# Kernel tuning notes

Hardware: AMD Instinct MI355X
Metric: run time of the kernel (lower is better)

Reference implementation:

```python
import jax, jax.numpy as jnp
import numpy as np

B, N, C, K = 8, 4096, 64, 30
EPS_BN = 1e-5
TINY = 1e-20  # guards sqrt/atan2 at the exact self-neighbor (rel == 0)


def _knn(p, k):
    xx = jnp.sum(p * p, axis=1)  # [B, N]
    pd = 2.0 * jnp.einsum('bdn,bdm->bnm', p, p) - xx[:, :, None] - xx[:, None, :]
    return jax.lax.top_k(pd, k)[1]  # [B, N, k]


def _bn(h, g, b):
    # BatchNorm1d in training mode: biased batch stats over all dims but channel (last)
    mu = jnp.mean(h, axis=(0, 1, 2), keepdims=True)
    var = jnp.var(h, axis=(0, 1, 2), keepdims=True)
    return (h - mu) * jax.lax.rsqrt(var + EPS_BN) * g + b


def _forward(x_loc, x, W1, g1, b1, W2, g2, b2, W3, g3, b3, k):
    Bsz = x.shape[0]
    idx = _knn(x_loc, k)                       # [B, N, k]
    bidx = jnp.arange(Bsz)[:, None, None]
    pts = x_loc.transpose(0, 2, 1)             # [B, N, 3]
    rel = pts[bidx, idx] - pts[:, :, None, :]  # [B, N, k, 3] neighbor - center
    xr, yr, zr = rel[..., 0], rel[..., 1], rel[..., 2]
    sxy2 = xr * xr + yr * yr
    r2 = sxy2 + zr * zr
    rho = jnp.sqrt(jnp.maximum(r2, TINY))
    sxy = jnp.sqrt(jnp.maximum(sxy2, TINY))
    deg_r = r2 < TINY
    deg_p = sxy2 < TINY
    theta = jnp.arctan2(jnp.where(deg_r, 0.0, zr), jnp.where(deg_r, 1.0, sxy))
    phi = jnp.arctan2(jnp.where(deg_p, 0.0, yr), jnp.where(deg_p, 1.0, xr))
    sph = jnp.stack([rho, theta, phi], axis=-1)            # [B, N, k, 3]
    # torch car2sph averages across the 3 spherical channels (dim=-1)
    feat = jnp.concatenate([sph, sph - jnp.mean(sph, axis=-1, keepdims=True)], axis=-1)  # [B,N,k,6]
    lrelu = lambda h: jax.nn.leaky_relu(h, 0.2)
    h = lrelu(_bn(feat @ W1.T, g1, b1))        # [B, N, k, 6]
    h = lrelu(_bn(h @ W2.T, g2, b2))           # [B, N, k, 3]
    h = lrelu(_bn(h @ W3.T, g3, b3))           # [B, N, k, 1]
    att = jax.nn.softmax(h[..., 0], axis=-1)   # [B, N, k]
    xk = x.transpose(0, 2, 1)[bidx, idx]       # [B, N, k, C]
    agg = jnp.einsum('bnkc,bnk->bnc', xk, att)
    return x + agg.transpose(0, 2, 1)          # [B, C, N]


def setup_inputs() -> dict:
    key = jax.random.key(0)
    ks = jax.random.split(key, 12)
    return {
        'x_loc': jax.random.normal(ks[0], (B, 3, N), jnp.float32),
        'x': jax.random.normal(ks[1], (B, C, N), jnp.float32),
        'W1': jax.random.normal(ks[2], (6, 6), jnp.float32) * 0.4,
        'g1': 1.0 + 0.1 * jax.random.normal(ks[3], (6,), jnp.float32),
        'b1': 0.1 * jax.random.normal(ks[4], (6,), jnp.float32),
        'W2': jax.random.normal(ks[5], (3, 6), jnp.float32) * 0.4,
        'g2': 1.0 + 0.1 * jax.random.normal(ks[6], (3,), jnp.float32),
        'b2': 0.1 * jax.random.normal(ks[7], (3,), jnp.float32),
        'W3': jax.random.normal(ks[8], (1, 3), jnp.float32) * 0.4,
        'g3': 1.0 + 0.1 * jax.random.normal(ks[9], (1,), jnp.float32),
        'b3': 0.1 * jax.random.normal(ks[10], (1,), jnp.float32),
        'k': K,
    }


def reference(x_loc, x, W1, g1, b1, W2, g2, b2, W3, g3, b3, k):
    return _forward(x_loc, x, W1, g1, b1, W2, g2, b2, W3, g3, b3, k)
```

## Files before the change

kernel.cpp:

```cpp
#include <hip/hip_runtime.h>
#include <math.h>

#define NPTS 4096
#define NB   8
#define NC   64
#define KSEL 30
#define NROWS (NB * NPTS * KSEL)
#define CNT_F 983040.0f
#define SURVZ 3840
#define P23_BLOCKS 960
#define P23_STRIDE (P23_BLOCKS * 256)

static __device__ __forceinline__ unsigned long long shfl_xor_u64(unsigned long long v, int lx) {
    int lo = __shfl_xor((int)(unsigned)(v & 0xFFFFFFFFULL), lx, 64);
    int hi = __shfl_xor((int)(unsigned)(v >> 32), lx, 64);
    return ((unsigned long long)(unsigned)hi << 32) | (unsigned)lo;
}

template <int NM>
static __device__ __forceinline__ void slot_reduce(const float* __restrict__ acc,
                                                   float* __restrict__ sSum, int tid) {
    if (tid < 64) {
        float pm[NM];
#pragma unroll
        for (int m = 0; m < NM; ++m) pm[m] = acc[m * 64 + tid];
#pragma unroll
        for (int o = 32; o > 0; o >>= 1) {
#pragma unroll
            for (int m = 0; m < NM; ++m) pm[m] += __shfl_xor(pm[m], o, 64);
        }
        if (tid == 0) {
#pragma unroll
            for (int m = 0; m < NM; ++m) sSum[m] = pm[m];
        }
    }
}

static __device__ __forceinline__ void bn1_params(const float* __restrict__ sSum,
                                                  const float* __restrict__ W1,
                                                  const float* __restrict__ g1,
                                                  const float* __restrict__ b1,
                                                  float* __restrict__ sPar, int tid) {
    if (tid < 6) {
        const float invN = 1.0f / CNT_F;
        const float m0 = sSum[0] * invN, m1 = sSum[1] * invN, m2 = sSum[2] * invN;
        const float E00 = sSum[3] * invN, E01 = sSum[4] * invN, E02 = sSum[5] * invN;
        const float E11 = sSum[6] * invN, E12 = sSum[7] * invN, E22 = sSum[8] * invN;
        const float* w = W1 + tid * 6;
        const float third = (w[3] + w[4] + w[5]) * (1.0f / 3.0f);
        const float a0 = w[0] + w[3] - third;
        const float a1 = w[1] + w[4] - third;
        const float a2 = w[2] + w[5] - third;
        const float mu = a0 * m0 + a1 * m1 + a2 * m2;
        const float E2 = a0 * a0 * E00 + a1 * a1 * E11 + a2 * a2 * E22 +
                         2.0f * (a0 * a1 * E01 + a0 * a2 * E02 + a1 * a2 * E12);
        const float var = E2 - mu * mu;
        const float sc = g1[tid] / sqrtf(var + 1e-5f);
        sPar[tid] = sc;
        sPar[6 + tid] = b1[tid] - mu * sc;
    }
}

static __device__ __forceinline__ void bn2_params(const float* __restrict__ sSum,
                                                  const float* __restrict__ W2,
                                                  const float* __restrict__ g2,
                                                  const float* __restrict__ b2,
                                                  float* __restrict__ sPar, int tid) {
    if (tid < 3) {
        const float invN = 1.0f / CNT_F;
        float Eh[6];
#pragma unroll
        for (int d = 0; d < 6; ++d) Eh[d] = sSum[d] * invN;
        float M[6][6];
        int q = 6;
#pragma unroll
        for (int a2 = 0; a2 < 6; ++a2)
#pragma unroll
            for (int b2_ = a2; b2_ < 6; ++b2_) {
                const float v = sSum[q++] * invN;
                M[a2][b2_] = v; M[b2_][a2] = v;
            }
        const float* w = W2 + tid * 6;
        float mu = 0.0f;
#pragma unroll
        for (int d = 0; d < 6; ++d) mu += w[d] * Eh[d];
        float E2 = 0.0f;
#pragma unroll
        for (int a2 = 0; a2 < 6; ++a2)
#pragma unroll
            for (int b2_ = 0; b2_ < 6; ++b2_) E2 += w[a2] * w[b2_] * M[a2][b2_];
        const float var = E2 - mu * mu;
        const float sc = g2[tid] / sqrtf(var + 1e-5f);
        sPar[12 + tid] = sc;
        sPar[15 + tid] = b2[tid] - mu * sc;
    }
}

static __device__ __forceinline__ void bn3_params(const float* __restrict__ sSum,
                                                  const float* __restrict__ W3,
                                                  const float* __restrict__ g3,
                                                  const float* __restrict__ b3,
                                                  float* __restrict__ sPar, int tid) {
    if (tid == 0) {
        const float invN = 1.0f / CNT_F;
        const float Eh0 = sSum[0] * invN, Eh1 = sSum[1] * invN, Eh2 = sSum[2] * invN;
        const float M00 = sSum[3] * invN, M01 = sSum[4] * invN, M02 = sSum[5] * invN;
        const float M11 = sSum[6] * invN, M12 = sSum[7] * invN, M22 = sSum[8] * invN;
        const float w0 = W3[0], w1 = W3[1], w2 = W3[2];
        const float mu = w0 * Eh0 + w1 * Eh1 + w2 * Eh2;
        const float E2 = w0 * w0 * M00 + w1 * w1 * M11 + w2 * w2 * M22 +
                         2.0f * (w0 * w1 * M01 + w0 * w2 * M02 + w1 * w2 * M12);
        const float var = E2 - mu * mu;
        const float sc = g3[0] / sqrtf(var + 1e-5f);
        sPar[0] = sc;
        sPar[1] = b3[0] - mu * sc;
    }
}

static __device__ __forceinline__ void mlp_h1(float s0, float s1, float s2,
                                              const float* __restrict__ W1,
                                              const float* __restrict__ sPar,
                                              float* __restrict__ h1) {
    const float mean = (s0 + s1 + s2) * (1.0f / 3.0f);
    const float f[6] = {s0, s1, s2, s0 - mean, s1 - mean, s2 - mean};
#pragma unroll
    for (int c = 0; c < 6; ++c) {
        float a = 0.0f;
#pragma unroll
        for (int d = 0; d < 6; ++d) a = fmaf(W1[c * 6 + d], f[d], a);
        const float z = fmaf(a, sPar[c], sPar[6 + c]);
        h1[c] = z >= 0.0f ? z : 0.2f * z;
    }
}

static __device__ __forceinline__ void mlp_h2(const float* __restrict__ h1,
                                              const float* __restrict__ W2,
                                              const float* __restrict__ sPar,
                                              float* __restrict__ h2) {
#pragma unroll
    for (int c = 0; c < 3; ++c) {
        float a = 0.0f;
#pragma unroll
        for (int d = 0; d < 6; ++d) a = fmaf(W2[c * 6 + d], h1[d], a);
        const float z = fmaf(a, sPar[12 + c], sPar[15 + c]);
        h2[c] = z >= 0.0f ? z : 0.2f * z;
    }
}

__global__ __launch_bounds__(512, 4) void knn_k(const float* __restrict__ xloc,
                                                int* __restrict__ idx_out,
                                                float* __restrict__ sph,
                                                float* __restrict__ accM) {
    __shared__ float4 pts[NPTS];
    __shared__ float msc[72];

    const int tid  = threadIdx.x;
    const int lane = tid & 63;
    const int wv   = tid >> 6;
    const int b    = blockIdx.y;
    const int n    = (blockIdx.x << 3) + wv;

    const float* xb = xloc + (size_t)b * (3 * NPTS);
    for (int i = tid; i < NPTS; i += 512) {
        const float x = xb[i], y = xb[NPTS + i], z = xb[2 * NPTS + i];
        const float xx = __fadd_rn(__fadd_rn(__fmul_rn(x, x), __fmul_rn(y, y)), __fmul_rn(z, z));
        pts[i] = make_float4(x, y, z, xx);
    }
    __syncthreads();

    const float4 q = pts[n];

    unsigned K[64];
    unsigned lm = 0;
#pragma unroll
    for (int t = 0; t < 64; ++t) {
        const float4 c = pts[lane + (t << 6)];
        const float dt = __fadd_rn(__fadd_rn(__fmul_rn(q.x, c.x), __fmul_rn(q.y, c.y)), __fmul_rn(q.z, c.z));
        const float pd = __fsub_rn(__fsub_rn(__fmul_rn(2.0f, dt), q.w), c.w);
        const unsigned u = __float_as_uint(pd);
        const unsigned key = u ^ ((unsigned)((int)u >> 31) | 0x80000000u);
        K[t] = key;
        lm = key > lm ? key : lm;
    }

    unsigned v = lm;
#pragma unroll
    for (int k = 2; k <= 64; k <<= 1) {
#pragma unroll
        for (int j2 = k >> 1; j2 > 0; j2 >>= 1) {
            const unsigned o = (unsigned)__shfl_xor((int)v, j2, 64);
            const bool keepmax = ((lane & j2) == 0) == ((lane & k) == 0);
            const unsigned mx = v > o ? v : o;
            const unsigned mn = v > o ? o : v;
            v = keepmax ? mx : mn;
        }
    }
    const unsigned tau = (unsigned)__shfl((int)v, 30, 64);

    __syncthreads();

    unsigned long long* surv = ((unsigned long long*)(pts + SURVZ)) + (wv << 6);
    surv[lane] = 0ULL;

    unsigned total = 0;
#pragma unroll
    for (int t = 0; t < 64; ++t) {
        const bool p = (K[t] >= tau);
        const unsigned long long m = __ballot(p);
        if (p) {
            const unsigned pos = total + (unsigned)__popcll(m & ((1ULL << lane) - 1ULL));
            if (pos < 64u) {
                const unsigned j = (unsigned)(lane + (t << 6));
                surv[pos] = ((unsigned long long)K[t] << 32) | (unsigned)(~j);
            }
        }
        total += (unsigned)__popcll(m);
    }
    __threadfence_block();

    const int bn = (b << 12) + n;
    const size_t obase = (size_t)bn * KSEL;
    int jn = 0;

    if (total <= 64u) {
        unsigned long long s = surv[lane];
#pragma unroll
        for (int k = 2; k <= 64; k <<= 1) {
#pragma unroll
            for (int j2 = k >> 1; j2 > 0; j2 >>= 1) {
                const unsigned long long o = shfl_xor_u64(s, j2);
                const bool keepmax = ((lane & j2) == 0) == ((lane & k) == 0);
                const unsigned long long mx = s > o ? s : o;
                const unsigned long long mn = s > o ? o : s;
                s = keepmax ? mx : mn;
            }
        }
        jn = (int)(~(unsigned)s) & (NPTS - 1);
        if (lane >= KSEL) jn = 0;
    } else {
        unsigned P = 0;
        for (int bit = 31; bit >= 0; --bit) {
            const unsigned cand = P | (1u << bit);
            int c = 0;
#pragma unroll
            for (int t = 0; t < 64; ++t) c += (K[t] >= cand) ? 1 : 0;
#pragma unroll
            for (int o = 32; o > 0; o >>= 1) c += __shfl_xor(c, o, 64);
            if (c >= KSEL) P = cand;
        }
        int* sj = (int*)surv;
        int emitted = 0;
#pragma unroll
        for (int t = 0; t < 64; ++t) {
            const bool g = (K[t] > P);
            const unsigned long long m = __ballot(g);
            if (g) {
                const int pos = emitted + (int)__popcll(m & ((1ULL << lane) - 1ULL));
                if (pos < KSEL) sj[pos] = lane + (t << 6);
            }
            emitted += (int)__popcll(m);
        }
#pragma unroll
        for (int t = 0; t < 64; ++t) {
            const bool e_ = (K[t] == P);
            const unsigned long long m = __ballot(e_);
            const int before = (int)__popcll(m & ((1ULL << lane) - 1ULL));
            if (e_ && (emitted + before) < KSEL) sj[emitted + before] = lane + (t << 6);
            emitted += (int)__popcll(m);
        }
        __threadfence_block();
        if (lane < KSEL) jn = sj[lane];
    }

    float s0 = 0.0f, s1 = 0.0f, s2 = 0.0f;
    if (lane < KSEL) {
        idx_out[obase + lane] = jn;
        float cx, cy, cz;
        if (jn >= SURVZ) {
            cx = xb[jn]; cy = xb[NPTS + jn]; cz = xb[2 * NPTS + jn];
        } else {
            const float4 c = pts[jn];
            cx = c.x; cy = c.y; cz = c.z;
        }
        const float xr = cx - q.x, yr = cy - q.y, zr = cz - q.z;
        const float sxy2 = xr * xr + yr * yr;
        const float r2   = sxy2 + zr * zr;
        const float rho  = sqrtf(fmaxf(r2, 1e-20f));
        const float sxy  = sqrtf(fmaxf(sxy2, 1e-20f));
        const bool dr = r2 < 1e-20f;
        const bool dp = sxy2 < 1e-20f;
        const float theta = atan2f(dr ? 0.0f : zr, dr ? 1.0f : sxy);
        const float phi   = atan2f(dp ? 0.0f : yr, dp ? 1.0f : xr);
        sph[obase + lane]             = rho;
        sph[NROWS + obase + lane]     = theta;
        sph[2 * NROWS + obase + lane] = phi;
        s0 = rho; s1 = theta; s2 = phi;
    }

    float mom[9] = {s0, s1, s2, s0 * s0, s0 * s1, s0 * s2, s1 * s1, s1 * s2, s2 * s2};
#pragma unroll
    for (int o = 32; o > 0; o >>= 1) {
#pragma unroll
        for (int m = 0; m < 9; ++m) mom[m] += __shfl_xor(mom[m], o, 64);
    }
    if (lane == 0) {
#pragma unroll
        for (int m = 0; m < 9; ++m) msc[wv * 9 + m] = mom[m];
    }
    __syncthreads();
    if (tid < 9) {
        float t_ = 0.0f;
#pragma unroll
        for (int w = 0; w < 8; ++w) t_ += msc[w * 9 + tid];
        atomicAdd(&accM[tid * 64 + ((blockIdx.y * 512 + blockIdx.x) & 63)], t_);
    }
}

__global__ __launch_bounds__(256) void p2_k(const float* __restrict__ sph,
                                            const float* __restrict__ x,
                                            float* __restrict__ xT,
                                            const float* __restrict__ W1,
                                            const float* __restrict__ g1,
                                            const float* __restrict__ b1,
                                            const float* __restrict__ accM,
                                            float* __restrict__ acc2) {
    __shared__ float sSum[9];
    __shared__ float sPar[12];
    __shared__ float red[4][27];
    __shared__ float tile[64][65];
    const int tid = threadIdx.x;
    slot_reduce<9>(accM, sSum, tid);
    __syncthreads();
    bn1_params(sSum, W1, g1, b1, sPar, tid);
    __syncthreads();

    float m27[27];
#pragma unroll
    for (int m = 0; m < 27; ++m) m27[m] = 0.0f;
#pragma unroll
    for (int s = 0; s < 4; ++s) {
        const size_t r = (size_t)blockIdx.x * 256 + tid + (size_t)s * P23_STRIDE;
        const float s0 = sph[r], s1 = sph[NROWS + r], s2 = sph[2 * NROWS + r];
        float h1[6];
        mlp_h1(s0, s1, s2, W1, sPar, h1);
        int qq = 6;
#pragma unroll
        for (int a2 = 0; a2 < 6; ++a2) {
            m27[a2] += h1[a2];
#pragma unroll
            for (int b2_ = a2; b2_ < 6; ++b2_) m27[qq++] += h1[a2] * h1[b2_];
        }
    }
#pragma unroll
    for (int o = 32; o > 0; o >>= 1) {
#pragma unroll
        for (int m = 0; m < 27; ++m) m27[m] += __shfl_xor(m27[m], o, 64);
    }
    const int lane = tid & 63, wv = tid >> 6;
    if (lane == 0) {
#pragma unroll
        for (int m = 0; m < 27; ++m) red[wv][m] = m27[m];
    }
    __syncthreads();
    if (tid < 27) {
        const float v = red[0][tid] + red[1][tid] + red[2][tid] + red[3][tid];
        atomicAdd(&acc2[tid * 64 + (blockIdx.x & 63)], v);
    }

    if (blockIdx.x < 512) {
        const int b  = blockIdx.x >> 6;
        const int n0 = (blockIdx.x & 63) << 6;
        const int tx = tid & 63;
        const int ty = tid >> 6;
        const float* xb = x + ((size_t)b << 18);
#pragma unroll
        for (int i = 0; i < 16; ++i) {
            const int c = (i << 2) + ty;
            tile[c][tx] = xb[((size_t)c << 12) + n0 + tx];
        }
        __syncthreads();
        float* ob = xT + ((size_t)b << 18);
#pragma unroll
        for (int i = 0; i < 16; ++i) {
            const int nl = (i << 2) + ty;
            ob[((size_t)(n0 + nl) << 6) + tx] = tile[tx][nl];
        }
    }
}

__global__ __launch_bounds__(256) void p3_k(const float* __restrict__ sph,
                                            const float* __restrict__ W1,
                                            const float* __restrict__ g1,
                                            const float* __restrict__ b1,
                                            const float* __restrict__ W2,
                                            const float* __restrict__ g2,
                                            const float* __restrict__ b2,
                                            const float* __restrict__ W3,
                                            const float* __restrict__ accM,
                                            const float* __restrict__ acc2,
                                            float* __restrict__ acc3,
                                            float* __restrict__ y3) {
    __shared__ float sSum[27];
    __shared__ float sPar[18];
    __shared__ float red[4][9];
    const int tid = threadIdx.x;
    slot_reduce<9>(accM, sSum, tid);
    __syncthreads();
    bn1_params(sSum, W1, g1, b1, sPar, tid);
    __syncthreads();
    slot_reduce<27>(acc2, sSum, tid);
    __syncthreads();
    bn2_params(sSum, W2, g2, b2, sPar, tid);
    __syncthreads();

    const float w30 = W3[0], w31 = W3[1], w32 = W3[2];

    float m9[9];
#pragma unroll
    for (int m = 0; m < 9; ++m) m9[m] = 0.0f;
#pragma unroll
    for (int s = 0; s < 4; ++s) {
        const size_t r = (size_t)blockIdx.x * 256 + tid + (size_t)s * P23_STRIDE;
        const float s0 = sph[r], s1 = sph[NROWS + r], s2 = sph[2 * NROWS + r];
        float h1[6], h2[3];
        mlp_h1(s0, s1, s2, W1, sPar, h1);
        mlp_h2(h1, W2, sPar, h2);
        y3[r] = fmaf(w30, h2[0], fmaf(w31, h2[1], w32 * h2[2]));
        m9[0] += h2[0]; m9[1] += h2[1]; m9[2] += h2[2];
        m9[3] += h2[0] * h2[0]; m9[4] += h2[0] * h2[1]; m9[5] += h2[0] * h2[2];
        m9[6] += h2[1] * h2[1]; m9[7] += h2[1] * h2[2]; m9[8] += h2[2] * h2[2];
    }
#pragma unroll
    for (int o = 32; o > 0; o >>= 1) {
#pragma unroll
        for (int m = 0; m < 9; ++m) m9[m] += __shfl_xor(m9[m], o, 64);
    }
    const int lane = tid & 63, wv = tid >> 6;
    if (lane == 0) {
#pragma unroll
        for (int m = 0; m < 9; ++m) red[wv][m] = m9[m];
    }
    __syncthreads();
    if (tid < 9) {
        const float v = red[0][tid] + red[1][tid] + red[2][tid] + red[3][tid];
        atomicAdd(&acc3[tid * 64 + (blockIdx.x & 63)], v);
    }
}

__global__ __launch_bounds__(256) void p4_k(const float* __restrict__ y3,
                                            const int* __restrict__ idx,
                                            const float* __restrict__ x,
                                            const float* __restrict__ xT,
                                            const float* __restrict__ W3,
                                            const float* __restrict__ g3,
                                            const float* __restrict__ b3,
                                            const float* __restrict__ acc3,
                                            float* __restrict__ out) {
    __shared__ float sSum[9];
    __shared__ float sPar[2];
    __shared__ float agg[32][65];
    const int tid = threadIdx.x;
    slot_reduce<9>(acc3, sSum, tid);
    __syncthreads();
    bn3_params(sSum, W3, g3, b3, sPar, tid);
    __syncthreads();
    const float sc3 = sPar[0], tb3 = sPar[1];

    const int lane = tid & 63, wv = tid >> 6;
    const int b    = blockIdx.x & 7;
    const int n0   = (blockIdx.x >> 3) << 5;
    const int p0   = (b << 12) + n0;
    const float* xTb = xT + ((size_t)b << 18);

    for (int i = 0; i < 8; ++i) {
        const int pl = (wv << 3) + i;
        const int p  = p0 + pl;
        float a = -3.4e38f;
        int jn = 0;
        if (lane < KSEL) {
            const size_t r = (size_t)p * KSEL + lane;
            const float z = fmaf(y3[r], sc3, tb3);
            a = z >= 0.0f ? z : 0.2f * z;
            jn = idx[r];
        }
        float mx = a;
#pragma unroll
        for (int o = 32; o > 0; o >>= 1) mx = fmaxf(mx, __shfl_xor(mx, o, 64));
        const float e = (lane < KSEL) ? expf(a - mx) : 0.0f;
        float se = e;
#pragma unroll
        for (int o = 32; o > 0; o >>= 1) se += __shfl_xor(se, o, 64);
        const float w = e / se;

        float acc0 = 0.0f, acc1 = 0.0f, acc2_ = 0.0f;
#pragma unroll
        for (int t = 0; t < KSEL; t += 3) {
            const int   j0 = __shfl(jn, t, 64);
            const float w0 = __shfl(w, t, 64);
            const int   j1 = __shfl(jn, t + 1, 64);
            const float w1 = __shfl(w, t + 1, 64);
            const int   j2 = __shfl(jn, t + 2, 64);
            const float w2 = __shfl(w, t + 2, 64);
            acc0  = fmaf(w0, xTb[((size_t)j0 << 6) + lane], acc0);
            acc1  = fmaf(w1, xTb[((size_t)j1 << 6) + lane], acc1);
            acc2_ = fmaf(w2, xTb[((size_t)j2 << 6) + lane], acc2_);
        }
        agg[pl][lane] = acc0 + acc1 + acc2_;
    }
    __syncthreads();

    const float* xb = x + ((size_t)b << 18);
    float* ob = out + ((size_t)b << 18);
    const int nl = tid & 31, cb = tid >> 5;
#pragma unroll
    for (int i = 0; i < 8; ++i) {
        const int c = (i << 3) + cb;
        const size_t off = ((size_t)c << 12) + n0 + nl;
        ob[off] = xb[off] + agg[nl][c];
    }
}

extern "C" void kernel_launch(void* const* d_in, const int* in_sizes, int n_in,
                              void* d_out, int out_size, void* d_ws, size_t ws_size,
                              hipStream_t stream) {
    const float* x_loc = (const float*)d_in[0];
    const float* x     = (const float*)d_in[1];
    const float* W1    = (const float*)d_in[2];
    const float* g1    = (const float*)d_in[3];
    const float* b1    = (const float*)d_in[4];
    const float* W2    = (const float*)d_in[5];
    const float* g2    = (const float*)d_in[6];
    const float* b2    = (const float*)d_in[7];
    const float* W3    = (const float*)d_in[8];
    const float* g3    = (const float*)d_in[9];
    const float* b3    = (const float*)d_in[10];
    float* out = (float*)d_out;

    float* accM = (float*)d_ws;
    float* acc2 = accM + 576;
    float* acc3 = acc2 + 1728;
    float* sph  = acc3 + 576;
    int*   idx  = (int*)(sph + 3 * (size_t)NROWS);
    float* y3   = (float*)(idx + NROWS);
    float* xT   = y3 + NROWS;

    hipMemsetAsync(d_ws, 0, 11520, stream);

    knn_k<<<dim3(NPTS / 8, NB), 512, 0, stream>>>(x_loc, idx, sph, accM);
    p2_k<<<P23_BLOCKS, 256, 0, stream>>>(sph, x, xT, W1, g1, b1, accM, acc2);
    p3_k<<<P23_BLOCKS, 256, 0, stream>>>(sph, W1, g1, b1, W2, g2, b2, W3, accM, acc2, acc3, y3);
    p4_k<<<(NB * NPTS) / 32, 256, 0, stream>>>(y3, idx, x, xT, W3, g3, b3, acc3, out);
}
```

Measured before the change: 254.2 us.

## Use ballot-based radix threshold in kNN and vectorize softmax aggregation gathers

The kNN kernel replaces the 64-lane bitonic sort used to find the 31st-largest per-lane maximum with a 32-step ballot/popcount radix search. Survivor selection now compares floats and only converts to sortable keys when a value is stored. Prefix counts use the mbcnt intrinsics. In the aggregation kernel, each wave gathers neighbor feature rows as float4 across four neighbor groups and then reduces them with cross-lane shuffles, cutting the number of load instructions. The risks are the extra shuffle reduction and the r8 loop covering t up to 31 while only 30 neighbors exist, which relies on lanes 30 and 31 carrying zero weight.

```diff
diff --git a/kernel.cpp b/kernel.cpp
--- a/kernel.cpp
+++ b/kernel.cpp
@@ -15,6 +15,11 @@
     int lo = __shfl_xor((int)(unsigned)(v & 0xFFFFFFFFULL), lx, 64);
     int hi = __shfl_xor((int)(unsigned)(v >> 32), lx, 64);
     return ((unsigned long long)(unsigned)hi << 32) | (unsigned)lo;
+}
+
+static __device__ __forceinline__ unsigned mbcnt64(unsigned long long m) {
+    return __builtin_amdgcn_mbcnt_hi((unsigned)(m >> 32),
+           __builtin_amdgcn_mbcnt_lo((unsigned)m, 0u));
 }
 
 template <int NM>
@@ -171,31 +176,27 @@
     const float4 q = pts[n];
 
     unsigned K[64];
-    unsigned lm = 0;
+    float lm = -3.402823466e38f;
 #pragma unroll
     for (int t = 0; t < 64; ++t) {
         const float4 c = pts[lane + (t << 6)];
         const float dt = __fadd_rn(__fadd_rn(__fmul_rn(q.x, c.x), __fmul_rn(q.y, c.y)), __fmul_rn(q.z, c.z));
         const float pd = __fsub_rn(__fsub_rn(__fmul_rn(2.0f, dt), q.w), c.w);
-        const unsigned u = __float_as_uint(pd);
-        const unsigned key = u ^ ((unsigned)((int)u >> 31) | 0x80000000u);
-        K[t] = key;
-        lm = key > lm ? key : lm;
-    }
-
-    unsigned v = lm;
-#pragma unroll
-    for (int k = 2; k <= 64; k <<= 1) {
-#pragma unroll
-        for (int j2 = k >> 1; j2 > 0; j2 >>= 1) {
-            const unsigned o = (unsigned)__shfl_xor((int)v, j2, 64);
-            const bool keepmax = ((lane & j2) == 0) == ((lane & k) == 0);
-            const unsigned mx = v > o ? v : o;
-            const unsigned mn = v > o ? o : v;
-            v = keepmax ? mx : mn;
-        }
-    }
-    const unsigned tau = (unsigned)__shfl((int)v, 30, 64);
+        K[t] = __float_as_uint(pd);
+        lm = fmaxf(lm, pd);
+    }
+
+    const unsigned ulm = __float_as_uint(lm);
+    const unsigned lmk = ulm ^ ((unsigned)((int)ulm >> 31) | 0x80000000u);
+    unsigned P31 = 0u;
+#pragma unroll
+    for (int bit = 31; bit >= 0; --bit) {
+        const unsigned cand = P31 | (1u << bit);
+        const int c = __popcll(__ballot(lmk >= cand));
+        P31 = (c >= 31) ? cand : P31;
+    }
+    const unsigned tu = (P31 & 0x80000000u) ? (P31 ^ 0x80000000u) : ~P31;
+    const float tauf = __uint_as_float(tu);
 
     __syncthreads();
 
@@ -205,16 +206,20 @@
     unsigned total = 0;
 #pragma unroll
     for (int t = 0; t < 64; ++t) {
-        const bool p = (K[t] >= tau);
+        const bool p = (__uint_as_float(K[t]) >= tauf);
         const unsigned long long m = __ballot(p);
-        if (p) {
-            const unsigned pos = total + (unsigned)__popcll(m & ((1ULL << lane) - 1ULL));
-            if (pos < 64u) {
-                const unsigned j = (unsigned)(lane + (t << 6));
-                surv[pos] = ((unsigned long long)K[t] << 32) | (unsigned)(~j);
+        if (m) {
+            if (p) {
+                const unsigned pos = total + mbcnt64(m);
+                if (pos < 64u) {
+                    const unsigned u = K[t];
+                    const unsigned key = u ^ ((unsigned)((int)u >> 31) | 0x80000000u);
+                    const unsigned j = (unsigned)(lane + (t << 6));
+                    surv[pos] = ((unsigned long long)key << 32) | (unsigned)(~j);
+                }
             }
-        }
-        total += (unsigned)__popcll(m);
+            total += (unsigned)__popcll(m);
+        }
     }
     __threadfence_block();
 
@@ -238,6 +243,11 @@
         jn = (int)(~(unsigned)s) & (NPTS - 1);
         if (lane >= KSEL) jn = 0;
     } else {
+#pragma unroll
+        for (int t = 0; t < 64; ++t) {
+            const unsigned u = K[t];
+            K[t] = u ^ ((unsigned)((int)u >> 31) | 0x80000000u);
+        }
         unsigned P = 0;
         for (int bit = 31; bit >= 0; --bit) {
             const unsigned cand = P | (1u << bit);
@@ -255,7 +265,7 @@
             const bool g = (K[t] > P);
             const unsigned long long m = __ballot(g);
             if (g) {
-                const int pos = emitted + (int)__popcll(m & ((1ULL << lane) - 1ULL));
+                const int pos = emitted + (int)mbcnt64(m);
                 if (pos < KSEL) sj[pos] = lane + (t << 6);
             }
             emitted += (int)__popcll(m);
@@ -264,7 +274,7 @@
         for (int t = 0; t < 64; ++t) {
             const bool e_ = (K[t] == P);
             const unsigned long long m = __ballot(e_);
-            const int before = (int)__popcll(m & ((1ULL << lane) - 1ULL));
+            const int before = (int)mbcnt64(m);
             if (e_ && (emitted + before) < KSEL) sj[emitted + before] = lane + (t << 6);
             emitted += (int)__popcll(m);
         }
@@ -471,6 +481,8 @@
     const int n0   = (blockIdx.x >> 3) << 5;
     const int p0   = (b << 12) + n0;
     const float* xTb = xT + ((size_t)b << 18);
+    const int g  = lane >> 4;
+    const int c4 = (lane & 15) << 2;
 
     for (int i = 0; i < 8; ++i) {
         const int pl = (wv << 3) + i;
@@ -492,20 +504,24 @@
         for (int o = 32; o > 0; o >>= 1) se += __shfl_xor(se, o, 64);
         const float w = e / se;
 
-        float acc0 = 0.0f, acc1 = 0.0f, acc2_ = 0.0f;
-#pragma unroll
-        for (int t = 0; t < KSEL; t += 3) {
-            const int   j0 = __shfl(jn, t, 64);
-            const float w0 = __shfl(w, t, 64);
-            const int   j1 = __shfl(jn, t + 1, 64);
-            const float w1 = __shfl(w, t + 1, 64);
-            const int   j2 = __shfl(jn, t + 2, 64);
-            const float w2 = __shfl(w, t + 2, 64);
-            acc0  = fmaf(w0, xTb[((size_t)j0 << 6) + lane], acc0);
-            acc1  = fmaf(w1, xTb[((size_t)j1 << 6) + lane], acc1);
-            acc2_ = fmaf(w2, xTb[((size_t)j2 << 6) + lane], acc2_);
-        }
-        agg[pl][lane] = acc0 + acc1 + acc2_;
+        float ax = 0.0f, ay = 0.0f, az = 0.0f, aw = 0.0f;
+#pragma unroll
+        for (int r8 = 0; r8 < 8; ++r8) {
+            const int t = (r8 << 2) + g;
+            const int   j  = __shfl(jn, t, 64);
+            const float wt = __shfl(w,  t, 64);
+            const float4 v = *reinterpret_cast<const float4*>(xTb + ((size_t)j << 6) + c4);
+            ax = fmaf(wt, v.x, ax); ay = fmaf(wt, v.y, ay);
+            az = fmaf(wt, v.z, az); aw = fmaf(wt, v.w, aw);
+        }
+        ax += __shfl_xor(ax, 32, 64); ay += __shfl_xor(ay, 32, 64);
+        az += __shfl_xor(az, 32, 64); aw += __shfl_xor(aw, 32, 64);
+        ax += __shfl_xor(ax, 16, 64); ay += __shfl_xor(ay, 16, 64);
+        az += __shfl_xor(az, 16, 64); aw += __shfl_xor(aw, 16, 64);
+        if (g == 0) {
+            agg[pl][c4]     = ax; agg[pl][c4 + 1] = ay;
+            agg[pl][c4 + 2] = az; agg[pl][c4 + 3] = aw;
+        }
     }
     __syncthreads();
 
```

Result: faster. 239.2 us (-5.9%).
